# Kernel optimization log

Hardware: AMD Instinct MI355X
Metric: run time of the kernel (lower is better)

The kernel has to match this reference:

```python
import jax, jax.numpy as jnp
import numpy as np

B, S, D = 2, 2048, 4096
H, KVH, HD = 32, 8, 128
WIN = 1024  # sliding window
THETA = 10000.0


def setup_inputs() -> dict:
    key = jax.random.key(0)
    ks = jax.random.split(key, 5)
    x = jax.random.normal(ks[0], (B, S, D), jnp.float32) * 0.02
    wq = jax.random.normal(ks[1], (H * HD, D), jnp.float32) * 0.02
    wk = jax.random.normal(ks[2], (KVH * HD, D), jnp.float32) * 0.02
    wv = jax.random.normal(ks[3], (KVH * HD, D), jnp.float32) * 0.02
    wo = jax.random.normal(ks[4], (D, H * HD), jnp.float32) * 0.02
    positions = jnp.arange(S, dtype=jnp.int32)
    inv_freq = 1.0 / (THETA ** (jnp.arange(0, HD, 2, dtype=jnp.float32) / HD))
    ang = positions.astype(jnp.float32)[:, None] * inv_freq[None, :]  # [S, HD/2]
    cos, sin = jnp.cos(ang), jnp.sin(ang)
    i = jnp.arange(S)[:, None]
    j = jnp.arange(S)[None, :]
    allowed = (j <= i) & (i - j < WIN)  # causal + sliding window
    mask = jnp.where(allowed, 0.0, -1e9).astype(jnp.float32)  # [S, S]
    return {"x": x, "wq": wq, "wk": wk, "wv": wv, "wo": wo,
            "cos": cos, "sin": sin, "mask": mask, "positions": positions}


def _apply_rope(t, cos, sin):
    # t: [B, S, nH, HD]; pairs are consecutive dims (torch view_as_complex layout)
    tr = t.reshape(t.shape[:-1] + (HD // 2, 2))
    t0, t1 = tr[..., 0], tr[..., 1]
    c = cos[None, :, None, :]
    s = sin[None, :, None, :]
    out = jnp.stack([t0 * c - t1 * s, t0 * s + t1 * c], axis=-1)
    return out.reshape(t.shape)


def reference(x, wq, wk, wv, wo, cos, sin, mask, positions):
    bsz, seqlen, _ = x.shape
    xq = (x @ wq.T).reshape(bsz, seqlen, H, HD)
    xk = (x @ wk.T).reshape(bsz, seqlen, KVH, HD)
    xv = (x @ wv.T).reshape(bsz, seqlen, KVH, HD)
    xq = _apply_rope(xq, cos, sin)
    xk = _apply_rope(xk, cos, sin)
    # GQA: repeat_kv head broadcast (prefill path: positions.size(0) > 1)
    rep = H // KVH
    key = jnp.repeat(xk, rep, axis=2)  # [B, S, H, HD]
    val = jnp.repeat(xv, rep, axis=2)
    q = xq.transpose(0, 2, 1, 3)  # [B, H, S, HD]
    k = key.transpose(0, 2, 1, 3)
    v = val.transpose(0, 2, 1, 3)
    scale = HD ** -0.5
    scores = jnp.einsum("bhqd,bhkd->bhqk", q, k) * scale
    scores = scores + mask[None, None, :, :]
    probs = jax.nn.softmax(scores.astype(jnp.float32), axis=-1).astype(q.dtype)
    out = jnp.einsum("bhqk,bhkd->bhqd", probs, v)
    out = out.transpose(0, 2, 1, 3).reshape(bsz, seqlen, H * HD)
    return out @ wo.T
```

## Files before the change

### kernel.cpp

```cpp
#include <hip/hip_runtime.h>
#include <hip/hip_bf16.h>

#define B_  2
#define S_  2048
#define D_  4096
#define H_  32
#define KVH_ 8
#define HD_ 128
#define WIN_ 1024

typedef __attribute__((ext_vector_type(8))) __bf16 bf16x8;
typedef __attribute__((ext_vector_type(4))) float f32x4;
using bf16 = __hip_bfloat16;

typedef const __attribute__((address_space(1))) void* gas_ptr;
typedef __attribute__((address_space(3))) void* las_ptr;

__device__ __forceinline__ void gload16(const void* g, void* l) {
    __builtin_amdgcn_global_load_lds((gas_ptr)g, (las_ptr)l, 16, 0, 0);
}

__device__ __forceinline__ bf16x8 load8(const bf16* p) {
    return *reinterpret_cast<const bf16x8*>(p);
}
__device__ __forceinline__ bf16x8 cvt8(const bf16* p) {
    return *reinterpret_cast<const bf16x8*>(p);
}
__device__ __forceinline__ bf16x8 cvt8(const float* p) {
    const float4* q = reinterpret_cast<const float4*>(p);
    float4 a = q[0], b = q[1];
    bf16x8 r;
    r[0] = (__bf16)a.x; r[1] = (__bf16)a.y; r[2] = (__bf16)a.z; r[3] = (__bf16)a.w;
    r[4] = (__bf16)b.x; r[5] = (__bf16)b.y; r[6] = (__bf16)b.z; r[7] = (__bf16)b.w;
    return r;
}
__device__ __forceinline__ void store1(float* p, float v) { *p = v; }
__device__ __forceinline__ void store1(bf16* p, float v) { *p = __float2bfloat16(v); }

__global__ __launch_bounds__(256) void cast_kernel(const float* __restrict__ in,
                                                   bf16* __restrict__ out) {
    long i = ((long)blockIdx.x * 256 + threadIdx.x) * 8;
    const float4* p = reinterpret_cast<const float4*>(in + i);
    float4 a = p[0], b = p[1];
    bf16x8 r;
    r[0] = (__bf16)a.x; r[1] = (__bf16)a.y; r[2] = (__bf16)a.z; r[3] = (__bf16)a.w;
    r[4] = (__bf16)b.x; r[5] = (__bf16)b.y; r[6] = (__bf16)b.z; r[7] = (__bf16)b.w;
    *reinterpret_cast<bf16x8*>(out + i) = r;
}

#define GBAR()  __builtin_amdgcn_s_barrier()
#define LGKM0() do { asm volatile("s_waitcnt lgkmcnt(0)" ::: "memory"); \
                     __builtin_amdgcn_sched_barrier(0); } while (0)
#define VMC(n)  do { asm volatile("s_waitcnt vmcnt(" #n ")" ::: "memory"); \
                     __builtin_amdgcn_sched_barrier(0); } while (0)

template <typename TC>
__global__ __launch_bounds__(512, 2) void gemm_nt_256(
    const bf16* __restrict__ A, const bf16* __restrict__ Bm,
    TC* __restrict__ C, int M, int N, int K) {
    __shared__ __bf16 lds[2][2][256 * 64];

    const int tid  = threadIdx.x;
    const int wave = tid >> 6;
    const int lane = tid & 63;
    const int col  = lane & 15;
    const int quad = lane >> 4;
    const int c7   = col & 7;
    const int wmi  = wave >> 2;
    const int wni  = wave & 3;
    const long m0  = (long)blockIdx.y * 256;
    const long n0  = (long)blockIdx.x * 256;
    const int  nt  = K >> 6;

    f32x4 zero = {0.f, 0.f, 0.f, 0.f};
    f32x4 acc[8][4];
#pragma unroll
    for (int i = 0; i < 8; i++)
#pragma unroll
        for (int j = 0; j < 4; j++) acc[i][j] = zero;

    long gA[4], gB[4];
    int  lofs[4];
#pragma unroll
    for (int j = 0; j < 4; j++) {
        int r  = j * 64 + wave * 8 + (lane >> 3);
        int cg = (lane & 7) ^ (r & 7);
        gA[j]   = (m0 + r) * (long)K + cg * 8;
        gB[j]   = (n0 + r) * (long)K + cg * 8;
        lofs[j] = (j * 64 + wave * 8) * 128;
    }

#pragma unroll
    for (int j = 0; j < 4; j++) {
        gload16(A  + gA[j], (char*)lds[0][0] + lofs[j]);
        gload16(Bm + gB[j], (char*)lds[0][1] + lofs[j]);
    }
    if (nt > 1) {
#pragma unroll
        for (int j = 0; j < 4; j++)
            gload16(Bm + gB[j] + 64, (char*)lds[1][1] + lofs[j]);
        gload16(A + gA[0] + 64, (char*)lds[1][0] + lofs[0]);
        gload16(A + gA[2] + 64, (char*)lds[1][0] + lofs[2]);
        VMC(6);
    } else {
        VMC(0);
    }
    GBAR();

#define RDA_(dst, mf, ks) \
    dst = *reinterpret_cast<const bf16x8*>(Ab + (wmi * 128 + (mf) * 16 + col) * 128 \
                                              + ((((ks) << 2) + quad) ^ c7) * 16)
#define MFMA16(mb) \
    do { \
        _Pragma("unroll") \
        for (int ks = 0; ks < 2; ks++) { \
            _Pragma("unroll") \
            for (int nf = 0; nf < 4; nf++) { \
                acc[mb][nf]     = __builtin_amdgcn_mfma_f32_16x16x32_bf16( \
                    a[0][ks], bfr[nf][ks], acc[mb][nf], 0, 0, 0); \
                acc[mb + 1][nf] = __builtin_amdgcn_mfma_f32_16x16x32_bf16( \
                    a[1][ks], bfr[nf][ks], acc[mb + 1][nf], 0, 0, 0); \
            } \
        } \
    } while (0)

    for (int t = 0; t < nt; ++t) {
        const int cur = t & 1;
        const char* Ab = (const char*)lds[cur][0];
        const char* Bb = (const char*)lds[cur][1];
        char* An2 = (char*)lds[cur ^ 1][0];
        char* Ac2 = (char*)lds[cur][0];
        char* Bc2 = (char*)lds[cur][1];

        bf16x8 bfr[4][2];
#pragma unroll
        for (int nf = 0; nf < 4; nf++)
#pragma unroll
            for (int ks = 0; ks < 2; ks++)
                bfr[nf][ks] = *reinterpret_cast<const bf16x8*>(
                    Bb + (wni * 64 + nf * 16 + col) * 128 + (((ks << 2) + quad) ^ c7) * 16);
        bf16x8 a[2][2];
        RDA_(a[0][0], 0, 0); RDA_(a[0][1], 0, 1);
        RDA_(a[1][0], 1, 0); RDA_(a[1][1], 1, 1);
        if (t + 1 < nt) {
            long ko = (long)(t + 1) * 64;
            gload16(A + gA[1] + ko, An2 + lofs[1]);
            gload16(A + gA[3] + ko, An2 + lofs[3]);
        }
        GBAR();
        LGKM0();
        __builtin_amdgcn_s_setprio(1);
        MFMA16(0);
        __builtin_amdgcn_s_setprio(0);
        GBAR();

        RDA_(a[0][0], 2, 0); RDA_(a[0][1], 2, 1);
        RDA_(a[1][0], 3, 0); RDA_(a[1][1], 3, 1);
        if (t + 2 < nt) {
            long ko = (long)(t + 2) * 64;
#pragma unroll
            for (int j = 0; j < 4; j++)
                gload16(Bm + gB[j] + ko, Bc2 + lofs[j]);
        }
        GBAR();
        LGKM0();
        __builtin_amdgcn_s_setprio(1);
        MFMA16(2);
        __builtin_amdgcn_s_setprio(0);
        GBAR();

        RDA_(a[0][0], 4, 0); RDA_(a[0][1], 4, 1);
        RDA_(a[1][0], 5, 0); RDA_(a[1][1], 5, 1);
        if (t + 2 < nt) {
            long ko = (long)(t + 2) * 64;
            gload16(A + gA[0] + ko, Ac2 + lofs[0]);
            gload16(A + gA[2] + ko, Ac2 + lofs[2]);
        }
        GBAR();
        LGKM0();
        __builtin_amdgcn_s_setprio(1);
        MFMA16(4);
        __builtin_amdgcn_s_setprio(0);
        GBAR();

        RDA_(a[0][0], 6, 0); RDA_(a[0][1], 6, 1);
        RDA_(a[1][0], 7, 0); RDA_(a[1][1], 7, 1);
        LGKM0();
        __builtin_amdgcn_s_setprio(1);
        MFMA16(6);
        __builtin_amdgcn_s_setprio(0);
        if (t + 2 < nt) { VMC(6); } else { VMC(0); }
        GBAR();
    }

#pragma unroll
    for (int mf = 0; mf < 8; mf++) {
#pragma unroll
        for (int nf = 0; nf < 4; nf++) {
            long row = m0 + wmi * 128 + mf * 16 + quad * 4;
            long cc  = n0 + wni * 64 + nf * 16 + col;
#pragma unroll
            for (int r = 0; r < 4; r++)
                store1(&C[(row + r) * (long)N + cc], acc[mf][nf][r]);
        }
    }
}

template <typename TC>
__global__ __launch_bounds__(256) void gemm_nt_fast(
    const bf16* __restrict__ A, const bf16* __restrict__ Bm,
    TC* __restrict__ C, int M, int N, int K) {
    __shared__ __bf16 As[128 * 64];
    __shared__ __bf16 Bs[128 * 64];

    const int tid  = threadIdx.x;
    const int wave = tid >> 6;
    const int lane = tid & 63;
    const int col  = lane & 15;
    const int quad = lane >> 4;
    const int c7   = col & 7;
    const int wm   = (wave >> 1) * 64;
    const int wn   = (wave & 1) * 64;
    const long m0  = (long)blockIdx.y * 128;
    const long n0  = (long)blockIdx.x * 128;

    f32x4 zero = {0.f, 0.f, 0.f, 0.f};
    f32x4 acc[4][4];
#pragma unroll
    for (int i = 0; i < 4; i++)
#pragma unroll
        for (int j = 0; j < 4; j++) acc[i][j] = zero;

    long goffA[4], goffB[4];
    int  loff[4];
#pragma unroll
    for (int i = 0; i < 4; i++) {
        int r  = (wave * 4 + i) * 8 + (lane >> 3);
        int cg = (lane & 7) ^ (r & 7);
        goffA[i] = (m0 + r) * (long)K + cg * 8;
        goffB[i] = (n0 + r) * (long)K + cg * 8;
        loff[i]  = (wave * 4 + i) * 1024;
    }

    for (int kt = 0; kt < K; kt += 64) {
#pragma unroll
        for (int i = 0; i < 4; i++) {
            gload16(A + goffA[i] + kt, (char*)As + loff[i]);
            gload16(Bm + goffB[i] + kt, (char*)Bs + loff[i]);
        }
        __syncthreads();

        bf16x8 af[2][4], bfv[2][4];
#pragma unroll
        for (int ks = 0; ks < 2; ks++) {
#pragma unroll
            for (int mt = 0; mt < 4; mt++) {
                int row = wm + mt * 16 + col;
                af[ks][mt] = *reinterpret_cast<const bf16x8*>(
                    (const char*)As + row * 128 + (((ks << 2) + quad) ^ c7) * 16);
            }
#pragma unroll
            for (int nt = 0; nt < 4; nt++) {
                int row = wn + nt * 16 + col;
                bfv[ks][nt] = *reinterpret_cast<const bf16x8*>(
                    (const char*)Bs + row * 128 + (((ks << 2) + quad) ^ c7) * 16);
            }
        }
#pragma unroll
        for (int ks = 0; ks < 2; ks++)
#pragma unroll
            for (int mt = 0; mt < 4; mt++)
#pragma unroll
                for (int nt = 0; nt < 4; nt++)
                    acc[mt][nt] = __builtin_amdgcn_mfma_f32_16x16x32_bf16(
                        af[ks][mt], bfv[ks][nt], acc[mt][nt], 0, 0, 0);
        __syncthreads();
    }

#pragma unroll
    for (int mt = 0; mt < 4; mt++) {
#pragma unroll
        for (int nt = 0; nt < 4; nt++) {
            long row = m0 + wm + mt * 16 + quad * 4;
            long cc  = n0 + wn + nt * 16 + col;
#pragma unroll
            for (int r = 0; r < 4; r++)
                store1(&C[(row + r) * (long)N + cc], acc[mt][nt][r]);
        }
    }
}

template <typename TA, typename TB, typename TC>
__global__ __launch_bounds__(256) void gemm_nt(
    const TA* __restrict__ A, const TB* __restrict__ Bm,
    TC* __restrict__ C, int M, int N, int K) {
    __shared__ __bf16 As[128 * 40];
    __shared__ __bf16 Bs[128 * 40];

    const int tid  = threadIdx.x;
    const int wave = tid >> 6;
    const int lane = tid & 63;
    const int col  = lane & 15;
    const int quad = lane >> 4;
    const int wm   = (wave >> 1) * 64;
    const int wn   = (wave & 1) * 64;
    const long m0  = (long)blockIdx.y * 128;
    const long n0  = (long)blockIdx.x * 128;

    f32x4 zero = {0.f, 0.f, 0.f, 0.f};
    f32x4 acc[4][4];
#pragma unroll
    for (int i = 0; i < 4; i++)
#pragma unroll
        for (int j = 0; j < 4; j++) acc[i][j] = zero;

    const int srow = tid >> 2;
    const int sch  = (tid & 3) * 8;

    for (int kt = 0; kt < K; kt += 32) {
        bf16x8 av0 = cvt8(A + (m0 + srow)      * (long)K + kt + sch);
        bf16x8 av1 = cvt8(A + (m0 + srow + 64) * (long)K + kt + sch);
        bf16x8 bv0 = cvt8(Bm + (n0 + srow)      * (long)K + kt + sch);
        bf16x8 bv1 = cvt8(Bm + (n0 + srow + 64) * (long)K + kt + sch);
        *reinterpret_cast<bf16x8*>(&As[srow * 40 + sch])        = av0;
        *reinterpret_cast<bf16x8*>(&As[(srow + 64) * 40 + sch]) = av1;
        *reinterpret_cast<bf16x8*>(&Bs[srow * 40 + sch])        = bv0;
        *reinterpret_cast<bf16x8*>(&Bs[(srow + 64) * 40 + sch]) = bv1;
        __syncthreads();

        bf16x8 af[4], bfv[4];
#pragma unroll
        for (int mt = 0; mt < 4; mt++)
            af[mt] = *reinterpret_cast<const bf16x8*>(&As[(wm + mt * 16 + col) * 40 + quad * 8]);
#pragma unroll
        for (int nt = 0; nt < 4; nt++)
            bfv[nt] = *reinterpret_cast<const bf16x8*>(&Bs[(wn + nt * 16 + col) * 40 + quad * 8]);
#pragma unroll
        for (int mt = 0; mt < 4; mt++)
#pragma unroll
            for (int nt = 0; nt < 4; nt++)
                acc[mt][nt] = __builtin_amdgcn_mfma_f32_16x16x32_bf16(
                    af[mt], bfv[nt], acc[mt][nt], 0, 0, 0);
        __syncthreads();
    }

#pragma unroll
    for (int mt = 0; mt < 4; mt++) {
#pragma unroll
        for (int nt = 0; nt < 4; nt++) {
            long row = m0 + wm + mt * 16 + quad * 4;
            long cc  = n0 + wn + nt * 16 + col;
#pragma unroll
            for (int r = 0; r < 4; r++)
                store1(&C[(row + r) * (long)N + cc], acc[mt][nt][r]);
        }
    }
}

__global__ void rope_kernel(bf16* __restrict__ t, const float* __restrict__ cosb,
                            const float* __restrict__ sinb, int nh, int total) {
    int idx = blockIdx.x * blockDim.x + threadIdx.x;
    if (idx >= total) return;
    int pair = idx & 63;
    int rest = idx >> 6;
    int hh   = rest % nh;
    int tok  = rest / nh;
    int s    = tok & (S_ - 1);
    long base = (long)tok * (nh * HD_) + hh * HD_ + pair * 2;
    float c  = cosb[s * 64 + pair];
    float sn = sinb[s * 64 + pair];
    float t0 = __bfloat162float(t[base]);
    float t1 = __bfloat162float(t[base + 1]);
    t[base]     = __float2bfloat16(t0 * c - t1 * sn);
    t[base + 1] = __float2bfloat16(t0 * sn + t1 * c);
}

__global__ __launch_bounds__(256) void transpose_v(const bf16* __restrict__ v,
                                                   bf16* __restrict__ vt) {
    __shared__ __bf16 tile[64][72];
    const int s0 = blockIdx.x * 64;
    const int d0 = blockIdx.y * 64;
    const int b  = blockIdx.z;
    const int tid = threadIdx.x;
    const int tr  = tid >> 3;
    const int c8  = (tid & 7) * 8;
#pragma unroll
    for (int p = 0; p < 2; p++) {
        int srow = tr + p * 32;
        bf16x8 val = load8(v + ((long)(b * S_ + s0 + srow)) * 1024 + d0 + c8);
        *reinterpret_cast<bf16x8*>(&tile[srow][c8]) = val;
    }
    __syncthreads();
#pragma unroll
    for (int p = 0; p < 2; p++) {
        int dd = tr + p * 32;
        bf16x8 ov;
#pragma unroll
        for (int j = 0; j < 8; j++) ov[j] = tile[c8 + j][dd];
        *reinterpret_cast<bf16x8*>(vt + ((long)(b * 1024 + d0 + dd)) * S_ + s0 + c8) = ov;
    }
}

__global__ __launch_bounds__(256) void attn_kernel(
    const bf16* __restrict__ q, const bf16* __restrict__ k,
    const bf16* __restrict__ vt, bf16* __restrict__ o) {
    const int qb  = blockIdx.x;
    const int h   = blockIdx.y;
    const int b   = blockIdx.z;
    const int tid = threadIdx.x;
    const int wave = tid >> 6;
    const int lane = tid & 63;
    const int col  = lane & 15;
    const int quad = lane >> 4;
    const int kvh  = h >> 2;
    const int i0   = qb * 64;
    const float scale = 0.08838834764831845f;

    __shared__ __bf16 Ks[64 * 128];
    __shared__ __bf16 Vs[128 * 64];
    __shared__ __bf16 Pl[4][16 * 72];

    bf16x8 qa[4];
    const bf16* qptr = q + ((long)(b * S_ + i0 + wave * 16 + col)) * (H_ * HD_)
                         + h * HD_ + quad * 8;
#pragma unroll
    for (int ks = 0; ks < 4; ks++) qa[ks] = load8(qptr + ks * 32);

    long gK[4], gV[4];
    int  lK[4], lV[4];
#pragma unroll
    for (int i = 0; i < 4; i++) {
        int rK  = (wave * 4 + i) * 4 + (lane >> 4);
        int cgK = (lane & 15) ^ (rK & 15);
        gK[i] = ((long)(b * S_) + rK) * (KVH_ * HD_) + kvh * HD_ + cgK * 8;
        lK[i] = (wave * 4 + i) * 1024;
        int rV  = (wave * 4 + i) * 8 + (lane >> 3);
        int cgV = (lane & 7) ^ (rV & 7);
        gV[i] = ((long)(b * 1024) + kvh * HD_ + rV) * (long)S_ + cgV * 8;
        lV[i] = (wave * 4 + i) * 1024;
    }

    f32x4 zero = {0.f, 0.f, 0.f, 0.f};
    f32x4 oacc[8];
#pragma unroll
    for (int i = 0; i < 8; i++) oacc[i] = zero;
    float lsum[4] = {0.f, 0.f, 0.f, 0.f};

    const int kb0 = (qb >= 16) ? (qb - 16) : 0;

    for (int kb = kb0; kb <= qb; kb++) {
#pragma unroll
        for (int i = 0; i < 4; i++) {
            gload16(k + gK[i] + (long)kb * 64 * (KVH_ * HD_), (char*)Ks + lK[i]);
            gload16(vt + gV[i] + kb * 64, (char*)Vs + lV[i]);
        }
        __syncthreads();

        f32x4 sfr[4];
#pragma unroll
        for (int nt = 0; nt < 4; nt++) {
            f32x4 s = zero;
            int row = nt * 16 + col;
#pragma unroll
            for (int ks = 0; ks < 4; ks++) {
                bf16x8 bfv = *reinterpret_cast<const bf16x8*>(
                    (const char*)Ks + row * 256 + (((ks << 2) + quad) ^ col) * 16);
                s = __builtin_amdgcn_mfma_f32_16x16x32_bf16(qa[ks], bfv, s, 0, 0, 0);
            }
            sfr[nt] = s;
        }
#pragma unroll
        for (int nt = 0; nt < 4; nt++) {
            int j = kb * 64 + nt * 16 + col;
#pragma unroll
            for (int r = 0; r < 4; r++) {
                int i = i0 + wave * 16 + quad * 4 + r;
                float p = 0.f;
                if (j <= i && (i - j) < WIN_) p = __expf(sfr[nt][r] * scale);
                lsum[r] += p;
                Pl[wave][(quad * 4 + r) * 72 + nt * 16 + col] = __float2bfloat16(p);
            }
        }
#pragma unroll
        for (int ks2 = 0; ks2 < 2; ks2++) {
            bf16x8 pa = *reinterpret_cast<const bf16x8*>(
                &Pl[wave][col * 72 + ks2 * 32 + quad * 8]);
#pragma unroll
            for (int nt2 = 0; nt2 < 8; nt2++) {
                int d = nt2 * 16 + col;
                bf16x8 vb = *reinterpret_cast<const bf16x8*>(
                    (const char*)Vs + d * 128 + ((((ks2 << 2) + quad)) ^ (col & 7)) * 16);
                oacc[nt2] = __builtin_amdgcn_mfma_f32_16x16x32_bf16(
                    pa, vb, oacc[nt2], 0, 0, 0);
            }
        }
        __syncthreads();
    }

#pragma unroll
    for (int m = 1; m < 16; m <<= 1) {
#pragma unroll
        for (int r = 0; r < 4; r++) lsum[r] += __shfl_xor(lsum[r], m, 64);
    }

    bf16* op = o + ((long)(b * S_ + i0 + wave * 16 + quad * 4)) * (H_ * HD_) + h * HD_;
#pragma unroll
    for (int nt2 = 0; nt2 < 8; nt2++) {
#pragma unroll
        for (int r = 0; r < 4; r++)
            op[(long)r * (H_ * HD_) + nt2 * 16 + col] =
                __float2bfloat16(oacc[nt2][r] / lsum[r]);
    }
}

extern "C" void kernel_launch(void* const* d_in, const int* in_sizes, int n_in,
                              void* d_out, int out_size, void* d_ws, size_t ws_size,
                              hipStream_t stream) {
    const float* x    = (const float*)d_in[0];
    const float* wq   = (const float*)d_in[1];
    const float* wk   = (const float*)d_in[2];
    const float* wv   = (const float*)d_in[3];
    const float* wo   = (const float*)d_in[4];
    const float* cosb = (const float*)d_in[5];
    const float* sinb = (const float*)d_in[6];
    float* out = (float*)d_out;

    const size_t T   = (size_t)B_ * S_;
    const size_t SZ_D  = T * (H_ * HD_);
    const size_t SZ_KV = T * (KVH_ * HD_);

    dim3 blk(256);
    const size_t need_fast = (SZ_D * 3 + SZ_KV * 3 + SZ_D) * 2;

    if (ws_size >= need_fast) {
        bf16* xb    = (bf16*)d_ws;
        bf16* wbuf  = xb    + SZ_D;
        bf16* q_ws  = wbuf  + SZ_D;
        bf16* k_ws  = q_ws  + SZ_D;
        bf16* v_ws  = k_ws  + SZ_KV;
        bf16* vt_ws = v_ws  + SZ_KV;
        bf16* ao_ws = vt_ws + SZ_KV;

        cast_kernel<<<SZ_D / 2048, blk, 0, stream>>>(x, xb);
        cast_kernel<<<SZ_D / 2048, blk, 0, stream>>>(wq, wbuf);
        gemm_nt_256<bf16><<<dim3(16, 16), dim3(512), 0, stream>>>(xb, wbuf, q_ws, 4096, 4096, 4096);
        cast_kernel<<<SZ_KV / 2048, blk, 0, stream>>>(wk, wbuf);
        gemm_nt_fast<bf16><<<dim3(8, 32), blk, 0, stream>>>(xb, wbuf, k_ws, 4096, 1024, 4096);
        cast_kernel<<<SZ_KV / 2048, blk, 0, stream>>>(wv, wbuf);
        gemm_nt_fast<bf16><<<dim3(8, 32), blk, 0, stream>>>(xb, wbuf, v_ws, 4096, 1024, 4096);

        rope_kernel<<<(B_ * S_ * H_ * 64 + 255) / 256, blk, 0, stream>>>(
            q_ws, cosb, sinb, H_, B_ * S_ * H_ * 64);
        rope_kernel<<<(B_ * S_ * KVH_ * 64 + 255) / 256, blk, 0, stream>>>(
            k_ws, cosb, sinb, KVH_, B_ * S_ * KVH_ * 64);
        transpose_v<<<dim3(32, 16, 2), blk, 0, stream>>>(v_ws, vt_ws);

        attn_kernel<<<dim3(32, 32, 2), blk, 0, stream>>>(q_ws, k_ws, vt_ws, ao_ws);

        cast_kernel<<<SZ_D / 2048, blk, 0, stream>>>(wo, wbuf);
        gemm_nt_256<float><<<dim3(16, 16), dim3(512), 0, stream>>>(ao_ws, wbuf, out, 4096, 4096, 4096);
    } else {
        bf16* q_ws  = (bf16*)d_ws;
        bf16* k_ws  = q_ws  + SZ_D;
        bf16* v_ws  = k_ws  + SZ_KV;
        bf16* vt_ws = v_ws  + SZ_KV;
        bf16* ao_ws = vt_ws + SZ_KV;

        gemm_nt<float, float, bf16><<<dim3(32, 32), blk, 0, stream>>>(x, wq, q_ws, 4096, 4096, 4096);
        gemm_nt<float, float, bf16><<<dim3(8, 32),  blk, 0, stream>>>(x, wk, k_ws, 4096, 1024, 4096);
        gemm_nt<float, float, bf16><<<dim3(8, 32),  blk, 0, stream>>>(x, wv, v_ws, 4096, 1024, 4096);

        rope_kernel<<<(B_ * S_ * H_ * 64 + 255) / 256, blk, 0, stream>>>(
            q_ws, cosb, sinb, H_, B_ * S_ * H_ * 64);
        rope_kernel<<<(B_ * S_ * KVH_ * 64 + 255) / 256, blk, 0, stream>>>(
            k_ws, cosb, sinb, KVH_, B_ * S_ * KVH_ * 64);
        transpose_v<<<dim3(32, 16, 2), blk, 0, stream>>>(v_ws, vt_ws);

        attn_kernel<<<dim3(32, 32, 2), blk, 0, stream>>>(q_ws, k_ws, vt_ws, ao_ws);

        gemm_nt<bf16, float, float><<<dim3(32, 32), blk, 0, stream>>>(ao_ws, wo, out, 4096, 4096, 4096);
    }
}
```

Measured before the change: 776.3 us.

## Double-buffer K/V tiles in attention kernel with async prefetch and wave priority

The attention kernel now keeps two LDS buffers for K and V and issues the global-to-LDS loads for the next key block before computing on the current one. It waits with explicit vmcnt counters and raw barriers instead of __syncthreads, so load latency can overlap the QK and PV MFMA work. It also raises wave priority around the MFMA sections. This doubles the K/V LDS footprint, which may reduce occupancy, and it relies on hand-set waitcnt values being correct.

```diff
diff --git a/kernel.cpp b/kernel.cpp
--- a/kernel.cpp
+++ b/kernel.cpp
@@ -36,6 +36,13 @@
 }
 __device__ __forceinline__ void store1(float* p, float v) { *p = v; }
 __device__ __forceinline__ void store1(bf16* p, float v) { *p = __float2bfloat16(v); }
+
+#define GBAR()  __builtin_amdgcn_s_barrier()
+#define SCB0()  __builtin_amdgcn_sched_barrier(0)
+#define LGKM0() do { asm volatile("s_waitcnt lgkmcnt(0)" ::: "memory"); \
+                     __builtin_amdgcn_sched_barrier(0); } while (0)
+#define VMC(n)  do { asm volatile("s_waitcnt vmcnt(" #n ")" ::: "memory"); \
+                     __builtin_amdgcn_sched_barrier(0); } while (0)
 
 __global__ __launch_bounds__(256) void cast_kernel(const float* __restrict__ in,
                                                    bf16* __restrict__ out) {
@@ -47,12 +54,6 @@
     r[4] = (__bf16)b.x; r[5] = (__bf16)b.y; r[6] = (__bf16)b.z; r[7] = (__bf16)b.w;
     *reinterpret_cast<bf16x8*>(out + i) = r;
 }
-
-#define GBAR()  __builtin_amdgcn_s_barrier()
-#define LGKM0() do { asm volatile("s_waitcnt lgkmcnt(0)" ::: "memory"); \
-                     __builtin_amdgcn_sched_barrier(0); } while (0)
-#define VMC(n)  do { asm volatile("s_waitcnt vmcnt(" #n ")" ::: "memory"); \
-                     __builtin_amdgcn_sched_barrier(0); } while (0)
 
 template <typename TC>
 __global__ __launch_bounds__(512, 2) void gemm_nt_256(
@@ -416,8 +417,8 @@
     const int i0   = qb * 64;
     const float scale = 0.08838834764831845f;
 
-    __shared__ __bf16 Ks[64 * 128];
-    __shared__ __bf16 Vs[128 * 64];
+    __shared__ __bf16 Ks[2][64 * 128];
+    __shared__ __bf16 Vs[2][128 * 64];
     __shared__ __bf16 Pl[4][16 * 72];
 
     bf16x8 qa[4];
@@ -448,15 +449,32 @@
 
     const int kb0 = (qb >= 16) ? (qb - 16) : 0;
 
+    VMC(0);
+
+#pragma unroll
+    for (int i = 0; i < 4; i++) {
+        gload16(k + gK[i] + (long)kb0 * 64 * (KVH_ * HD_), (char*)Ks[0] + lK[i]);
+        gload16(vt + gV[i] + kb0 * 64, (char*)Vs[0] + lV[i]);
+    }
+
     for (int kb = kb0; kb <= qb; kb++) {
-#pragma unroll
-        for (int i = 0; i < 4; i++) {
-            gload16(k + gK[i] + (long)kb * 64 * (KVH_ * HD_), (char*)Ks + lK[i]);
-            gload16(vt + gV[i] + kb * 64, (char*)Vs + lV[i]);
-        }
-        __syncthreads();
+        const int cur = (kb - kb0) & 1;
+        if (kb < qb) {
+#pragma unroll
+            for (int i = 0; i < 4; i++) {
+                gload16(k + gK[i] + (long)(kb + 1) * 64 * (KVH_ * HD_),
+                        (char*)Ks[cur ^ 1] + lK[i]);
+                gload16(vt + gV[i] + (kb + 1) * 64, (char*)Vs[cur ^ 1] + lV[i]);
+            }
+            VMC(8);
+        } else {
+            VMC(0);
+        }
+        GBAR();
+        SCB0();
 
         f32x4 sfr[4];
+        __builtin_amdgcn_s_setprio(1);
 #pragma unroll
         for (int nt = 0; nt < 4; nt++) {
             f32x4 s = zero;
@@ -464,11 +482,12 @@
 #pragma unroll
             for (int ks = 0; ks < 4; ks++) {
                 bf16x8 bfv = *reinterpret_cast<const bf16x8*>(
-                    (const char*)Ks + row * 256 + (((ks << 2) + quad) ^ col) * 16);
+                    (const char*)Ks[cur] + row * 256 + (((ks << 2) + quad) ^ col) * 16);
                 s = __builtin_amdgcn_mfma_f32_16x16x32_bf16(qa[ks], bfv, s, 0, 0, 0);
             }
             sfr[nt] = s;
         }
+        __builtin_amdgcn_s_setprio(0);
 #pragma unroll
         for (int nt = 0; nt < 4; nt++) {
             int j = kb * 64 + nt * 16 + col;
@@ -481,6 +500,7 @@
                 Pl[wave][(quad * 4 + r) * 72 + nt * 16 + col] = __float2bfloat16(p);
             }
         }
+        __builtin_amdgcn_s_setprio(1);
 #pragma unroll
         for (int ks2 = 0; ks2 < 2; ks2++) {
             bf16x8 pa = *reinterpret_cast<const bf16x8*>(
@@ -489,12 +509,14 @@
             for (int nt2 = 0; nt2 < 8; nt2++) {
                 int d = nt2 * 16 + col;
                 bf16x8 vb = *reinterpret_cast<const bf16x8*>(
-                    (const char*)Vs + d * 128 + ((((ks2 << 2) + quad)) ^ (col & 7)) * 16);
+                    (const char*)Vs[cur] + d * 128 + ((((ks2 << 2) + quad)) ^ (col & 7)) * 16);
                 oacc[nt2] = __builtin_amdgcn_mfma_f32_16x16x32_bf16(
                     pa, vb, oacc[nt2], 0, 0, 0);
             }
         }
-        __syncthreads();
+        __builtin_amdgcn_s_setprio(0);
+        GBAR();
+        SCB0();
     }
 
 #pragma unroll
```

After: 794.3 us. +2.3%, slower.

## Process 128 query rows per attention block to reuse K/V tiles

Applied to the files above, without the earlier changes.

The attention kernel now covers 128 query rows per block, with each wave handling two 16-row groups, so every K and V^T tile loaded into LDS feeds twice as many query rows. The grid along the query dimension is halved, and the key-block range is recomputed for the larger query tile. MFMA sections are wrapped in s_setprio raises, and the launch bounds request 3 blocks per CU. The cost is more registers per wave (two sets of Q fragments and output accumulators) and a larger P buffer in LDS, which could lower occupancy.

```diff
diff --git a/kernel.cpp b/kernel.cpp
--- a/kernel.cpp
+++ b/kernel.cpp
@@ -36,6 +36,13 @@
 }
 __device__ __forceinline__ void store1(float* p, float v) { *p = v; }
 __device__ __forceinline__ void store1(bf16* p, float v) { *p = __float2bfloat16(v); }
+
+#define GBAR()  __builtin_amdgcn_s_barrier()
+#define SCB0()  __builtin_amdgcn_sched_barrier(0)
+#define LGKM0() do { asm volatile("s_waitcnt lgkmcnt(0)" ::: "memory"); \
+                     __builtin_amdgcn_sched_barrier(0); } while (0)
+#define VMC(n)  do { asm volatile("s_waitcnt vmcnt(" #n ")" ::: "memory"); \
+                     __builtin_amdgcn_sched_barrier(0); } while (0)
 
 __global__ __launch_bounds__(256) void cast_kernel(const float* __restrict__ in,
                                                    bf16* __restrict__ out) {
@@ -47,12 +54,6 @@
     r[4] = (__bf16)b.x; r[5] = (__bf16)b.y; r[6] = (__bf16)b.z; r[7] = (__bf16)b.w;
     *reinterpret_cast<bf16x8*>(out + i) = r;
 }
-
-#define GBAR()  __builtin_amdgcn_s_barrier()
-#define LGKM0() do { asm volatile("s_waitcnt lgkmcnt(0)" ::: "memory"); \
-                     __builtin_amdgcn_sched_barrier(0); } while (0)
-#define VMC(n)  do { asm volatile("s_waitcnt vmcnt(" #n ")" ::: "memory"); \
-                     __builtin_amdgcn_sched_barrier(0); } while (0)
 
 template <typename TC>
 __global__ __launch_bounds__(512, 2) void gemm_nt_256(
@@ -401,7 +402,7 @@
     }
 }
 
-__global__ __launch_bounds__(256) void attn_kernel(
+__global__ __launch_bounds__(256, 3) void attn_kernel(
     const bf16* __restrict__ q, const bf16* __restrict__ k,
     const bf16* __restrict__ vt, bf16* __restrict__ o) {
     const int qb  = blockIdx.x;
@@ -413,18 +414,21 @@
     const int col  = lane & 15;
     const int quad = lane >> 4;
     const int kvh  = h >> 2;
-    const int i0   = qb * 64;
+    const int i0   = qb * 128;
     const float scale = 0.08838834764831845f;
 
     __shared__ __bf16 Ks[64 * 128];
     __shared__ __bf16 Vs[128 * 64];
-    __shared__ __bf16 Pl[4][16 * 72];
-
-    bf16x8 qa[4];
-    const bf16* qptr = q + ((long)(b * S_ + i0 + wave * 16 + col)) * (H_ * HD_)
-                         + h * HD_ + quad * 8;
-#pragma unroll
-    for (int ks = 0; ks < 4; ks++) qa[ks] = load8(qptr + ks * 32);
+    __shared__ __bf16 Pl[4][32 * 72];
+
+    bf16x8 qa[2][4];
+#pragma unroll
+    for (int mg = 0; mg < 2; mg++) {
+        const bf16* qptr = q + ((long)(b * S_ + i0 + wave * 32 + mg * 16 + col)) * (H_ * HD_)
+                             + h * HD_ + quad * 8;
+#pragma unroll
+        for (int ks = 0; ks < 4; ks++) qa[mg][ks] = load8(qptr + ks * 32);
+    }
 
     long gK[4], gV[4];
     int  lK[4], lV[4];
@@ -441,14 +445,17 @@
     }
 
     f32x4 zero = {0.f, 0.f, 0.f, 0.f};
-    f32x4 oacc[8];
-#pragma unroll
-    for (int i = 0; i < 8; i++) oacc[i] = zero;
-    float lsum[4] = {0.f, 0.f, 0.f, 0.f};
-
-    const int kb0 = (qb >= 16) ? (qb - 16) : 0;
-
-    for (int kb = kb0; kb <= qb; kb++) {
+    f32x4 oacc[2][8];
+#pragma unroll
+    for (int mg = 0; mg < 2; mg++)
+#pragma unroll
+        for (int i = 0; i < 8; i++) oacc[mg][i] = zero;
+    float lsum[2][4] = {{0.f, 0.f, 0.f, 0.f}, {0.f, 0.f, 0.f, 0.f}};
+
+    const int kb0 = (qb >= 8) ? (2 * qb - 16) : 0;
+    const int kbe = 2 * qb + 1;
+
+    for (int kb = kb0; kb <= kbe; kb++) {
 #pragma unroll
         for (int i = 0; i < 4; i++) {
             gload16(k + gK[i] + (long)kb * 64 * (KVH_ * HD_), (char*)Ks + lK[i]);
@@ -456,60 +463,72 @@
         }
         __syncthreads();
 
-        f32x4 sfr[4];
-#pragma unroll
-        for (int nt = 0; nt < 4; nt++) {
-            f32x4 s = zero;
-            int row = nt * 16 + col;
-#pragma unroll
-            for (int ks = 0; ks < 4; ks++) {
-                bf16x8 bfv = *reinterpret_cast<const bf16x8*>(
-                    (const char*)Ks + row * 256 + (((ks << 2) + quad) ^ col) * 16);
-                s = __builtin_amdgcn_mfma_f32_16x16x32_bf16(qa[ks], bfv, s, 0, 0, 0);
+#pragma unroll
+        for (int mg = 0; mg < 2; mg++) {
+            f32x4 sfr[4];
+            __builtin_amdgcn_s_setprio(1);
+#pragma unroll
+            for (int nt = 0; nt < 4; nt++) {
+                f32x4 s = zero;
+                int row = nt * 16 + col;
+#pragma unroll
+                for (int ks = 0; ks < 4; ks++) {
+                    bf16x8 bfv = *reinterpret_cast<const bf16x8*>(
+                        (const char*)Ks + row * 256 + (((ks << 2) + quad) ^ col) * 16);
+                    s = __builtin_amdgcn_mfma_f32_16x16x32_bf16(qa[mg][ks], bfv, s, 0, 0, 0);
+                }
+                sfr[nt] = s;
             }
-            sfr[nt] = s;
-        }
-#pragma unroll
-        for (int nt = 0; nt < 4; nt++) {
-            int j = kb * 64 + nt * 16 + col;
-#pragma unroll
-            for (int r = 0; r < 4; r++) {
-                int i = i0 + wave * 16 + quad * 4 + r;
-                float p = 0.f;
-                if (j <= i && (i - j) < WIN_) p = __expf(sfr[nt][r] * scale);
-                lsum[r] += p;
-                Pl[wave][(quad * 4 + r) * 72 + nt * 16 + col] = __float2bfloat16(p);
+            __builtin_amdgcn_s_setprio(0);
+#pragma unroll
+            for (int nt = 0; nt < 4; nt++) {
+                int j = kb * 64 + nt * 16 + col;
+#pragma unroll
+                for (int r = 0; r < 4; r++) {
+                    int i = i0 + wave * 32 + mg * 16 + quad * 4 + r;
+                    float p = 0.f;
+                    if (j <= i && (i - j) < WIN_) p = __expf(sfr[nt][r] * scale);
+                    lsum[mg][r] += p;
+                    Pl[wave][(mg * 16 + quad * 4 + r) * 72 + nt * 16 + col] = __float2bfloat16(p);
+                }
             }
-        }
-#pragma unroll
-        for (int ks2 = 0; ks2 < 2; ks2++) {
-            bf16x8 pa = *reinterpret_cast<const bf16x8*>(
-                &Pl[wave][col * 72 + ks2 * 32 + quad * 8]);
-#pragma unroll
-            for (int nt2 = 0; nt2 < 8; nt2++) {
-                int d = nt2 * 16 + col;
-                bf16x8 vb = *reinterpret_cast<const bf16x8*>(
-                    (const char*)Vs + d * 128 + ((((ks2 << 2) + quad)) ^ (col & 7)) * 16);
-                oacc[nt2] = __builtin_amdgcn_mfma_f32_16x16x32_bf16(
-                    pa, vb, oacc[nt2], 0, 0, 0);
+            __builtin_amdgcn_s_setprio(1);
+#pragma unroll
+            for (int ks2 = 0; ks2 < 2; ks2++) {
+                bf16x8 pa = *reinterpret_cast<const bf16x8*>(
+                    &Pl[wave][(mg * 16 + col) * 72 + ks2 * 32 + quad * 8]);
+#pragma unroll
+                for (int nt2 = 0; nt2 < 8; nt2++) {
+                    int d = nt2 * 16 + col;
+                    bf16x8 vb = *reinterpret_cast<const bf16x8*>(
+                        (const char*)Vs + d * 128 + ((((ks2 << 2) + quad)) ^ (col & 7)) * 16);
+                    oacc[mg][nt2] = __builtin_amdgcn_mfma_f32_16x16x32_bf16(
+                        pa, vb, oacc[mg][nt2], 0, 0, 0);
+                }
             }
+            __builtin_amdgcn_s_setprio(0);
         }
         __syncthreads();
     }
 
 #pragma unroll
-    for (int m = 1; m < 16; m <<= 1) {
-#pragma unroll
-        for (int r = 0; r < 4; r++) lsum[r] += __shfl_xor(lsum[r], m, 64);
-    }
-
-    bf16* op = o + ((long)(b * S_ + i0 + wave * 16 + quad * 4)) * (H_ * HD_) + h * HD_;
-#pragma unroll
-    for (int nt2 = 0; nt2 < 8; nt2++) {
-#pragma unroll
-        for (int r = 0; r < 4; r++)
-            op[(long)r * (H_ * HD_) + nt2 * 16 + col] =
-                __float2bfloat16(oacc[nt2][r] / lsum[r]);
+    for (int m = 1; m < 16; m <<= 1)
+#pragma unroll
+        for (int mg = 0; mg < 2; mg++)
+#pragma unroll
+            for (int r = 0; r < 4; r++) lsum[mg][r] += __shfl_xor(lsum[mg][r], m, 64);
+
+#pragma unroll
+    for (int mg = 0; mg < 2; mg++) {
+        bf16* op = o + ((long)(b * S_ + i0 + wave * 32 + mg * 16 + quad * 4)) * (H_ * HD_)
+                     + h * HD_;
+#pragma unroll
+        for (int nt2 = 0; nt2 < 8; nt2++) {
+#pragma unroll
+            for (int r = 0; r < 4; r++)
+                op[(long)r * (H_ * HD_) + nt2 * 16 + col] =
+                    __float2bfloat16(oacc[mg][nt2][r] / lsum[mg][r]);
+        }
     }
 }
 
@@ -555,7 +574,7 @@
             k_ws, cosb, sinb, KVH_, B_ * S_ * KVH_ * 64);
         transpose_v<<<dim3(32, 16, 2), blk, 0, stream>>>(v_ws, vt_ws);
 
-        attn_kernel<<<dim3(32, 32, 2), blk, 0, stream>>>(q_ws, k_ws, vt_ws, ao_ws);
+        attn_kernel<<<dim3(16, 32, 2), blk, 0, stream>>>(q_ws, k_ws, vt_ws, ao_ws);
 
         cast_kernel<<<SZ_D / 2048, blk, 0, stream>>>(wo, wbuf);
         gemm_nt_256<float><<<dim3(16, 16), dim3(512), 0, stream>>>(ao_ws, wbuf, out, 4096, 4096, 4096);
@@ -576,7 +595,7 @@
             k_ws, cosb, sinb, KVH_, B_ * S_ * KVH_ * 64);
         transpose_v<<<dim3(32, 16, 2), blk, 0, stream>>>(v_ws, vt_ws);
 
-        attn_kernel<<<dim3(32, 32, 2), blk, 0, stream>>>(q_ws, k_ws, vt_ws, ao_ws);
+        attn_kernel<<<dim3(16, 32, 2), blk, 0, stream>>>(q_ws, k_ws, vt_ws, ao_ws);
 
         gemm_nt<bf16, float, float><<<dim3(32, 32), blk, 0, stream>>>(ao_ws, wo, out, 4096, 4096, 4096);
     }
```

Measured after the change: 969.1 us. 1.25x slower.
